# Optimization experiments

Measured on AMD Instinct MI355X. Metric: run time of the kernel, lower is better.

The kernel has to match this reference:

```python
import jax, jax.numpy as jnp
import numpy as np

N_HEAD = 16
HEAD_SIZE = 1024
EMBED = 1024
MULTI_HEAD_SIZE = HEAD_SIZE // N_HEAD  # 64; used only as the softmax scale (source bug)
B, S = 4, 2048


def setup_inputs() -> dict:
    key = jax.random.key(0)
    k1, k2, k3, k4 = jax.random.split(key, 4)
    x = jax.random.normal(k1, (B, S, EMBED), dtype=jnp.float32)
    w_qkv = jax.random.normal(k2, (3 * HEAD_SIZE, EMBED), dtype=jnp.float32) * 0.02
    w_proj = jax.random.normal(k3, (EMBED, HEAD_SIZE), dtype=jnp.float32) * 0.02
    b_proj = jax.random.normal(k4, (EMBED,), dtype=jnp.float32) * 0.02
    return {"x": x, "w_qkv": w_qkv, "w_proj": w_proj, "b_proj": b_proj}


def reference(x, w_qkv, w_proj, b_proj):
    # Fused QKV projection (Linear, no bias): [B,S,E] @ [E,3H] -> split
    qkv = jnp.einsum("bse,he->bsh", x, w_qkv)  # [B,S,3H]
    q, k, v = jnp.split(qkv, 3, axis=-1)       # each [B,S,H]
    # Source's non-flash path: attention over FULL Head_size dim (not per-head),
    # scaled by sqrt(multi_head_size) -- reproduced faithfully.
    scale = 1.0 / np.sqrt(MULTI_HEAD_SIZE).astype(np.float32)
    scores = jnp.einsum("bqh,bkh->bqk", q, k) * scale  # [B,S,S]
    probs = jax.nn.softmax(scores, axis=-1)            # dropout = identity (eval)
    out = jnp.einsum("bqk,bkh->bqh", probs, v)         # [B,S,H]
    # Faithful scrambling reshape: transpose(1,2).contiguous().view(B,S,H)
    Bn, Sn, H = out.shape
    out = jnp.swapaxes(out, 1, 2).reshape(Bn, Sn, H)
    # Output projection + residual dropout (identity in eval)
    out = jnp.einsum("bsh,eh->bse", out, w_proj) + b_proj
    return out
```

## Files before the change

### kernel.cpp

```cpp
#include <hip/hip_runtime.h>


typedef float f32x4 __attribute__((ext_vector_type(4)));
typedef short bf16x8 __attribute__((ext_vector_type(8)));
typedef short bf16x4 __attribute__((ext_vector_type(4)));
typedef unsigned short u16;

__device__ inline u16 f2bf(float f) {
  union { float f; unsigned u; } x; x.f = f;
  unsigned r = x.u + 0x7fffu + ((x.u >> 16) & 1u);
  return (u16)(r >> 16);
}

__device__ inline void gload_lds16(const void* g, void* l) {
  __builtin_amdgcn_global_load_lds(
      (const __attribute__((address_space(1))) void*)g,
      (__attribute__((address_space(3))) void*)l, 16, 0, 0);
}

__global__ __launch_bounds__(256) void cvt_kernel(const float* __restrict__ in,
                                                  u16* __restrict__ out, int n8) {
  int i = blockIdx.x * 256 + threadIdx.x;
  if (i >= n8) return;
  f32x4 a = *(const f32x4*)&in[(long)i * 8];
  f32x4 b = *(const f32x4*)&in[(long)i * 8 + 4];
  bf16x8 o;
#pragma unroll
  for (int j = 0; j < 4; ++j) { o[j] = (short)f2bf(a[j]); o[4 + j] = (short)f2bf(b[j]); }
  *(bf16x8*)&out[(long)i * 8] = o;
}

__global__ __launch_bounds__(256) void transpose_v(const u16* __restrict__ qkvb,
                                                   u16* __restrict__ vT) {
  __shared__ u16 tile[64][72];
  const int t = threadIdx.x;
  const long b = blockIdx.z;
  const int k0 = blockIdx.x * 64, h0 = blockIdx.y * 64;
  const u16* v = qkvb + b * 2048 * 3072 + 2048;
#pragma unroll
  for (int i = 0; i < 2; ++i) {
    int s = i * 256 + t; int r = s >> 3, c = (s & 7) * 8;
    bf16x8 val = *(const bf16x8*)&v[(long)(k0 + r) * 3072 + h0 + c];
    *(bf16x8*)&tile[r][c] = val;
  }
  __syncthreads();
  u16* o = vT + b * 1024 * 2048;
#pragma unroll
  for (int i = 0; i < 2; ++i) {
    int s = i * 256 + t; int r = s >> 3, c = (s & 7) * 8;
    bf16x8 val;
#pragma unroll
    for (int j = 0; j < 8; ++j) val[j] = tile[c + j][r];
    *(bf16x8*)&o[(long)(h0 + r) * 2048 + k0 + c] = val;
  }
}

__global__ __launch_bounds__(256) void softmax_k(const float* __restrict__ S,
                                                 u16* __restrict__ P,
                                                 long sS, long sP) {
  const int t = threadIdx.x;
  const float* row = S + (long)blockIdx.z * sS + (long)blockIdx.x * 2048;
  u16* prow = P + (long)blockIdx.z * sP + (long)blockIdx.x * 2048;
  f32x4 v0 = *(const f32x4*)&row[t * 8];
  f32x4 v1 = *(const f32x4*)&row[t * 8 + 4];
  float m = v0[0];
#pragma unroll
  for (int j = 1; j < 4; ++j) m = fmaxf(m, v0[j]);
#pragma unroll
  for (int j = 0; j < 4; ++j) m = fmaxf(m, v1[j]);
#pragma unroll
  for (int o = 32; o; o >>= 1) m = fmaxf(m, __shfl_xor(m, o));
  __shared__ float red[8];
  if ((t & 63) == 0) red[t >> 6] = m;
  __syncthreads();
  m = fmaxf(fmaxf(red[0], red[1]), fmaxf(red[2], red[3]));
  const float C = 0.18033688011112042f;
  float e[8], s = 0.f;
#pragma unroll
  for (int j = 0; j < 4; ++j) { e[j] = exp2f((v0[j] - m) * C); s += e[j]; }
#pragma unroll
  for (int j = 0; j < 4; ++j) { e[4 + j] = exp2f((v1[j] - m) * C); s += e[4 + j]; }
#pragma unroll
  for (int o = 32; o; o >>= 1) s += __shfl_xor(s, o);
  if ((t & 63) == 0) red[4 + (t >> 6)] = s;
  __syncthreads();
  float inv = 1.f / (red[4] + red[5] + red[6] + red[7]);
  bf16x8 ov;
#pragma unroll
  for (int j = 0; j < 8; ++j) ov[j] = (short)f2bf(e[j] * inv);
  *(bf16x8*)&prow[t * 8] = ov;
}

template <int MODE, int BM>
__global__ __launch_bounds__(512, 2) void gemm9(const u16* __restrict__ A0, int lda, long sAz,
                                                const u16* __restrict__ B0, int ldb, long sBz,
                                                void* __restrict__ C0, int ldc, long sCz,
                                                const float* __restrict__ bias, int K) {
  constexpr int MR = BM / 32;
  constexpr int LA = BM / 128;
  extern __shared__ __align__(16) u16 smem[];
  u16* Ab = smem;
  u16* Bb = smem + 4 * BM * 32;
  const int t = threadIdx.x, lane = t & 63, wv = t >> 6;
  const int wr = wv >> 2, wc = wv & 3;
  const int fr = lane & 15, hi = lane >> 4;

  const int gx = gridDim.x, gy = gridDim.y;
  long L = ((long)blockIdx.z * gy + blockIdx.y) * gx + blockIdx.x;
  const long NB = (long)gx * gy * gridDim.z;
  if ((NB & 7) == 0) L = (L & 7) * (NB >> 3) + (L >> 3);
  const int bx = (int)(L % gx);
  const int by = (int)((L / gx) % gy);
  const int bz = (int)(L / ((long)gx * gy));

  const long row0 = (long)by * BM, col0 = (long)bx * 256;
  const u16* A = A0 + (long)bz * sAz;
  const u16* B = B0 + (long)bz * sBz;

  f32x4 acc[MR][4];
#pragma unroll
  for (int m = 0; m < MR; ++m)
#pragma unroll
    for (int n = 0; n < 4; ++n) acc[m][n] = (f32x4){0.f, 0.f, 0.f, 0.f};

  auto stA = [&](int buf, int ks, int k0) {
#pragma unroll
    for (int i = 0; i < LA; ++i) {
      const int l = i * 512 + t;
      const int r = l >> 2, sl = (l & 3) ^ (r & 3);
      gload_lds16(A + (row0 + r) * (long)lda + k0 + ks * 32 + sl * 8,
                  Ab + (buf * 2 + ks) * BM * 32 + (i * 512 + wv * 64) * 8);
    }
  };
  auto stB = [&](int buf, int ks, int k0) {
#pragma unroll
    for (int i = 0; i < 2; ++i) {
      const int l = i * 512 + t;
      const int r = l >> 2, sl = (l & 3) ^ (r & 3);
      gload_lds16(B + (col0 + r) * (long)ldb + k0 + ks * 32 + sl * 8,
                  Bb + (buf * 2 + ks) * 256 * 32 + (i * 512 + wv * 64) * 8);
    }
  };
  auto aAddr = [&](int buf, int ks, int m) -> const u16* {
    const int r = wr * (BM / 2) + m * 16 + fr;
    return Ab + ((buf * 2 + ks) * BM + r) * 32 + (hi ^ (fr & 3)) * 8;
  };
  auto bAddr = [&](int buf, int ks, int n) -> const u16* {
    const int r = wc * 64 + n * 16 + fr;
    return Bb + ((buf * 2 + ks) * 256 + r) * 32 + (hi ^ (fr & 3)) * 8;
  };

  stA(0, 0, 0); stB(0, 0, 0);
  stA(0, 1, 0); stB(0, 1, 0);

  const int NT = K >> 6;
  for (int kt = 0; kt < NT; ++kt) {
    const int buf = kt & 1;
    const int kn = (kt + 1) << 6;
    const bool pf = (kt + 1 < NT);
#pragma unroll
    for (int ks = 0; ks < 2; ++ks) {
      if constexpr (LA == 2) asm volatile("s_waitcnt vmcnt(4)" ::: "memory");
      else                   asm volatile("s_waitcnt vmcnt(3)" ::: "memory");
      __builtin_amdgcn_s_barrier();
      __builtin_amdgcn_sched_barrier(0);
      bf16x8 afr[MR], b01[2], b23[2];
#pragma unroll
      for (int m = 0; m < MR; ++m) afr[m] = *(const bf16x8*)aAddr(buf, ks, m);
#pragma unroll
      for (int n = 0; n < 2; ++n) b01[n] = *(const bf16x8*)bAddr(buf, ks, n);
#pragma unroll
      for (int n = 0; n < 2; ++n) b23[n] = *(const bf16x8*)bAddr(buf, ks, 2 + n);
      if (pf) { stA(buf ^ 1, ks, kn); stB(buf ^ 1, ks, kn); }
      asm volatile("s_waitcnt lgkmcnt(2)" ::: "memory");
      __builtin_amdgcn_sched_barrier(0);
      __builtin_amdgcn_s_setprio(1);
#pragma unroll
      for (int m = 0; m < MR; ++m) {
        acc[m][0] = __builtin_amdgcn_mfma_f32_16x16x32_bf16(afr[m], b01[0], acc[m][0], 0, 0, 0);
        acc[m][1] = __builtin_amdgcn_mfma_f32_16x16x32_bf16(afr[m], b01[1], acc[m][1], 0, 0, 0);
      }
      __builtin_amdgcn_s_setprio(0);
      asm volatile("s_waitcnt lgkmcnt(0)" ::: "memory");
      __builtin_amdgcn_sched_barrier(0);
      __builtin_amdgcn_s_setprio(1);
#pragma unroll
      for (int m = 0; m < MR; ++m) {
        acc[m][2] = __builtin_amdgcn_mfma_f32_16x16x32_bf16(afr[m], b23[0], acc[m][2], 0, 0, 0);
        acc[m][3] = __builtin_amdgcn_mfma_f32_16x16x32_bf16(afr[m], b23[1], acc[m][3], 0, 0, 0);
      }
      __builtin_amdgcn_s_setprio(0);
    }
  }

#pragma unroll
  for (int m = 0; m < MR; ++m)
#pragma unroll
    for (int n = 0; n < 4; ++n) {
      const long r0 = row0 + wr * (BM / 2) + m * 16 + hi * 4;
      const long c = col0 + wc * 64 + n * 16 + fr;
      if (MODE == 0) {
        float* C = (float*)C0 + (long)bz * sCz;
#pragma unroll
        for (int j = 0; j < 4; ++j) C[(r0 + j) * ldc + c] = acc[m][n][j];
      } else if (MODE == 1) {
        u16* C = (u16*)C0 + (long)bz * sCz;
#pragma unroll
        for (int j = 0; j < 4; ++j) C[(r0 + j) * ldc + c] = f2bf(acc[m][n][j]);
      } else if (MODE == 2) {
        u16* C = (u16*)C0 + (long)bz * sCz;
        const int q0 = (int)r0;
        const long dr = 2 * c + (q0 >> 10);
        bf16x4 pk;
#pragma unroll
        for (int j = 0; j < 4; ++j) pk[j] = (short)f2bf(acc[m][n][j]);
        *(bf16x4*)&C[dr * 1024 + (q0 & 1023)] = pk;
      } else {
        float* C = (float*)C0 + (long)bz * sCz;
        const float bv = bias[c];
#pragma unroll
        for (int j = 0; j < 4; ++j) C[(r0 + j) * ldc + c] = acc[m][n][j] + bv;
      }
    }
}

extern "C" void kernel_launch(void* const* d_in, const int* in_sizes, int n_in,
                              void* d_out, int out_size, void* d_ws, size_t ws_size,
                              hipStream_t stream) {
  const float* x      = (const float*)d_in[0];
  const float* w_qkv  = (const float*)d_in[1];
  const float* w_proj = (const float*)d_in[2];
  const float* b_proj = (const float*)d_in[3];
  float* out = (float*)d_out;
  char* ws = (char*)d_ws;

  u16*   xb     = (u16*)(ws + 0);
  u16*   wqkvb  = (u16*)(ws + 16777216);
  u16*   wprojb = (u16*)(ws + 23068672);
  u16*   qkvb   = (u16*)(ws + 25165824);
  u16*   vT     = (u16*)(ws + 75497472);
  u16*   out2   = (u16*)(ws + 92274688);
  float* scores = (float*)(ws + 109051904);
  const bool full = ws_size >= 209715200ull;
  u16* probs = (u16*)(ws + (full ? 176160768 : 125829120));

  const int LDS128 = (4 * 128 * 32 + 4 * 256 * 32) * 2;
  const int LDS256 = (4 * 256 * 32 + 4 * 256 * 32) * 2;
  hipFuncSetAttribute((const void*)gemm9<1, 128>, hipFuncAttributeMaxDynamicSharedMemorySize, LDS128);
  hipFuncSetAttribute((const void*)gemm9<0, 256>, hipFuncAttributeMaxDynamicSharedMemorySize, LDS256);
  hipFuncSetAttribute((const void*)gemm9<2, 128>, hipFuncAttributeMaxDynamicSharedMemorySize, LDS128);
  hipFuncSetAttribute((const void*)gemm9<3, 128>, hipFuncAttributeMaxDynamicSharedMemorySize, LDS128);

  cvt_kernel<<<4096, 256, 0, stream>>>(x, xb, 1048576);
  cvt_kernel<<<1536, 256, 0, stream>>>(w_qkv, wqkvb, 393216);
  cvt_kernel<<<512, 256, 0, stream>>>(w_proj, wprojb, 131072);

  gemm9<1, 128><<<dim3(12, 64, 1), 512, LDS128, stream>>>(xb, 1024, 0, wqkvb, 1024, 0,
                                                          qkvb, 3072, 0, nullptr, 1024);
  transpose_v<<<dim3(32, 16, 4), 256, 0, stream>>>(qkvb, vT);

  const long sQ = 2048L * 3072;
  if (full) {
    gemm9<0, 256><<<dim3(8, 8, 4), 512, LDS256, stream>>>(qkvb, 3072, sQ, qkvb + 1024, 3072, sQ,
                                                          scores, 2048, 2048L * 2048, nullptr, 1024);
    softmax_k<<<dim3(2048, 1, 4), 256, 0, stream>>>(scores, probs, 2048L * 2048, 2048L * 2048);
    gemm9<2, 128><<<dim3(4, 16, 4), 512, LDS128, stream>>>(probs, 2048, 2048L * 2048, vT, 2048, 2048L * 1024,
                                                           out2, 1024, 2048L * 1024, nullptr, 2048);
  } else {
    for (int b = 0; b < 4; ++b) {
      const u16* qb = qkvb + (long)b * sQ;
      gemm9<0, 256><<<dim3(8, 8, 1), 512, LDS256, stream>>>(qb, 3072, 0, qb + 1024, 3072, 0,
                                                            scores, 2048, 0, nullptr, 1024);
      softmax_k<<<dim3(2048, 1, 1), 256, 0, stream>>>(scores, probs, 0, 0);
      gemm9<2, 128><<<dim3(4, 16, 1), 512, LDS128, stream>>>(probs, 2048, 0, vT + (long)b * 2048 * 1024, 2048, 0,
                                                             out2 + (long)b * 2048 * 1024, 1024, 0, nullptr, 2048);
    }
  }

  gemm9<3, 128><<<dim3(4, 64, 1), 512, LDS128, stream>>>(out2, 1024, 0, wprojb, 1024, 0,
                                                         out, 1024, 0, b_proj, 1024);
}
```

Before: 295.3 us.

## Simplify GEMM main loop to single-stage K=32 with higher occupancy

Replaces the hand-scheduled two-substep K=64 pipeline with a simpler K=32 double-buffered loop using __syncthreads, drops the XOR LDS swizzle, halves LDS per block, and raises the launch-bounds occupancy hint (4 or 6 waves-groups). The QKV GEMM also moves to a 256-row tile. The aim is more concurrent blocks to hide latency instead of explicit waitcnt/setprio scheduling, at the risk of LDS bank conflicts from the unswizzled layout and more barriers per K step.

```diff
diff --git a/kernel.cpp b/kernel.cpp
--- a/kernel.cpp
+++ b/kernel.cpp
@@ -91,16 +91,16 @@
   *(bf16x8*)&prow[t * 8] = ov;
 }
 
-template <int MODE, int BM>
-__global__ __launch_bounds__(512, 2) void gemm9(const u16* __restrict__ A0, int lda, long sAz,
-                                                const u16* __restrict__ B0, int ldb, long sBz,
-                                                void* __restrict__ C0, int ldc, long sCz,
-                                                const float* __restrict__ bias, int K) {
+template <int MODE, int BM, int MINW>
+__global__ __launch_bounds__(512, MINW) void gemm10(const u16* __restrict__ A0, int lda, long sAz,
+                                                    const u16* __restrict__ B0, int ldb, long sBz,
+                                                    void* __restrict__ C0, int ldc, long sCz,
+                                                    const float* __restrict__ bias, int K) {
   constexpr int MR = BM / 32;
   constexpr int LA = BM / 128;
   extern __shared__ __align__(16) u16 smem[];
   u16* Ab = smem;
-  u16* Bb = smem + 4 * BM * 32;
+  u16* Bb = smem + 2 * BM * 32;
   const int t = threadIdx.x, lane = t & 63, wv = t >> 6;
   const int wr = wv >> 2, wc = wv & 3;
   const int fr = lane & 15, hi = lane >> 4;
@@ -123,74 +123,43 @@
 #pragma unroll
     for (int n = 0; n < 4; ++n) acc[m][n] = (f32x4){0.f, 0.f, 0.f, 0.f};
 
-  auto stA = [&](int buf, int ks, int k0) {
+  auto stage = [&](int buf, int k0) {
 #pragma unroll
     for (int i = 0; i < LA; ++i) {
       const int l = i * 512 + t;
-      const int r = l >> 2, sl = (l & 3) ^ (r & 3);
-      gload_lds16(A + (row0 + r) * (long)lda + k0 + ks * 32 + sl * 8,
-                  Ab + (buf * 2 + ks) * BM * 32 + (i * 512 + wv * 64) * 8);
-    }
-  };
-  auto stB = [&](int buf, int ks, int k0) {
+      const int r = l >> 2, sl = l & 3;
+      gload_lds16(A + (row0 + r) * (long)lda + k0 + sl * 8,
+                  Ab + buf * BM * 32 + (i * 512 + wv * 64) * 8);
+    }
 #pragma unroll
     for (int i = 0; i < 2; ++i) {
       const int l = i * 512 + t;
-      const int r = l >> 2, sl = (l & 3) ^ (r & 3);
-      gload_lds16(B + (col0 + r) * (long)ldb + k0 + ks * 32 + sl * 8,
-                  Bb + (buf * 2 + ks) * 256 * 32 + (i * 512 + wv * 64) * 8);
+      const int r = l >> 2, sl = l & 3;
+      gload_lds16(B + (col0 + r) * (long)ldb + k0 + sl * 8,
+                  Bb + buf * 256 * 32 + (i * 512 + wv * 64) * 8);
     }
   };
-  auto aAddr = [&](int buf, int ks, int m) -> const u16* {
-    const int r = wr * (BM / 2) + m * 16 + fr;
-    return Ab + ((buf * 2 + ks) * BM + r) * 32 + (hi ^ (fr & 3)) * 8;
-  };
-  auto bAddr = [&](int buf, int ks, int n) -> const u16* {
-    const int r = wc * 64 + n * 16 + fr;
-    return Bb + ((buf * 2 + ks) * 256 + r) * 32 + (hi ^ (fr & 3)) * 8;
-  };
-
-  stA(0, 0, 0); stB(0, 0, 0);
-  stA(0, 1, 0); stB(0, 1, 0);
-
-  const int NT = K >> 6;
+
+  stage(0, 0);
+  __syncthreads();
+
+  const int NT = K >> 5;
   for (int kt = 0; kt < NT; ++kt) {
-    const int buf = kt & 1;
-    const int kn = (kt + 1) << 6;
-    const bool pf = (kt + 1 < NT);
-#pragma unroll
-    for (int ks = 0; ks < 2; ++ks) {
-      if constexpr (LA == 2) asm volatile("s_waitcnt vmcnt(4)" ::: "memory");
-      else                   asm volatile("s_waitcnt vmcnt(3)" ::: "memory");
-      __builtin_amdgcn_s_barrier();
-      __builtin_amdgcn_sched_barrier(0);
-      bf16x8 afr[MR], b01[2], b23[2];
-#pragma unroll
-      for (int m = 0; m < MR; ++m) afr[m] = *(const bf16x8*)aAddr(buf, ks, m);
-#pragma unroll
-      for (int n = 0; n < 2; ++n) b01[n] = *(const bf16x8*)bAddr(buf, ks, n);
-#pragma unroll
-      for (int n = 0; n < 2; ++n) b23[n] = *(const bf16x8*)bAddr(buf, ks, 2 + n);
-      if (pf) { stA(buf ^ 1, ks, kn); stB(buf ^ 1, ks, kn); }
-      asm volatile("s_waitcnt lgkmcnt(2)" ::: "memory");
-      __builtin_amdgcn_sched_barrier(0);
-      __builtin_amdgcn_s_setprio(1);
-#pragma unroll
-      for (int m = 0; m < MR; ++m) {
-        acc[m][0] = __builtin_amdgcn_mfma_f32_16x16x32_bf16(afr[m], b01[0], acc[m][0], 0, 0, 0);
-        acc[m][1] = __builtin_amdgcn_mfma_f32_16x16x32_bf16(afr[m], b01[1], acc[m][1], 0, 0, 0);
-      }
-      __builtin_amdgcn_s_setprio(0);
-      asm volatile("s_waitcnt lgkmcnt(0)" ::: "memory");
-      __builtin_amdgcn_sched_barrier(0);
-      __builtin_amdgcn_s_setprio(1);
-#pragma unroll
-      for (int m = 0; m < MR; ++m) {
-        acc[m][2] = __builtin_amdgcn_mfma_f32_16x16x32_bf16(afr[m], b23[0], acc[m][2], 0, 0, 0);
-        acc[m][3] = __builtin_amdgcn_mfma_f32_16x16x32_bf16(afr[m], b23[1], acc[m][3], 0, 0, 0);
-      }
-      __builtin_amdgcn_s_setprio(0);
-    }
+    const int cur = kt & 1;
+    if (kt + 1 < NT) stage(cur ^ 1, (kt + 1) << 5);
+    bf16x8 afr[MR], bfr[4];
+#pragma unroll
+    for (int m = 0; m < MR; ++m)
+      afr[m] = *(const bf16x8*)(Ab + (cur * BM + wr * (BM / 2) + m * 16 + fr) * 32 + hi * 8);
+#pragma unroll
+    for (int n = 0; n < 4; ++n)
+      bfr[n] = *(const bf16x8*)(Bb + (cur * 256 + wc * 64 + n * 16 + fr) * 32 + hi * 8);
+#pragma unroll
+    for (int m = 0; m < MR; ++m)
+#pragma unroll
+      for (int n = 0; n < 4; ++n)
+        acc[m][n] = __builtin_amdgcn_mfma_f32_16x16x32_bf16(afr[m], bfr[n], acc[m][n], 0, 0, 0);
+    __syncthreads();
   }
 
 #pragma unroll
@@ -244,39 +213,39 @@
   const bool full = ws_size >= 209715200ull;
   u16* probs = (u16*)(ws + (full ? 176160768 : 125829120));
 
-  const int LDS128 = (4 * 128 * 32 + 4 * 256 * 32) * 2;
-  const int LDS256 = (4 * 256 * 32 + 4 * 256 * 32) * 2;
-  hipFuncSetAttribute((const void*)gemm9<1, 128>, hipFuncAttributeMaxDynamicSharedMemorySize, LDS128);
-  hipFuncSetAttribute((const void*)gemm9<0, 256>, hipFuncAttributeMaxDynamicSharedMemorySize, LDS256);
-  hipFuncSetAttribute((const void*)gemm9<2, 128>, hipFuncAttributeMaxDynamicSharedMemorySize, LDS128);
-  hipFuncSetAttribute((const void*)gemm9<3, 128>, hipFuncAttributeMaxDynamicSharedMemorySize, LDS128);
+  const int L256 = (2 * 256 * 32 + 2 * 256 * 32) * 2;
+  const int L128 = (2 * 128 * 32 + 2 * 256 * 32) * 2;
+  hipFuncSetAttribute((const void*)gemm10<1, 256, 4>, hipFuncAttributeMaxDynamicSharedMemorySize, L256);
+  hipFuncSetAttribute((const void*)gemm10<0, 256, 4>, hipFuncAttributeMaxDynamicSharedMemorySize, L256);
+  hipFuncSetAttribute((const void*)gemm10<2, 128, 6>, hipFuncAttributeMaxDynamicSharedMemorySize, L128);
+  hipFuncSetAttribute((const void*)gemm10<3, 128, 6>, hipFuncAttributeMaxDynamicSharedMemorySize, L128);
 
   cvt_kernel<<<4096, 256, 0, stream>>>(x, xb, 1048576);
   cvt_kernel<<<1536, 256, 0, stream>>>(w_qkv, wqkvb, 393216);
   cvt_kernel<<<512, 256, 0, stream>>>(w_proj, wprojb, 131072);
 
-  gemm9<1, 128><<<dim3(12, 64, 1), 512, LDS128, stream>>>(xb, 1024, 0, wqkvb, 1024, 0,
-                                                          qkvb, 3072, 0, nullptr, 1024);
+  gemm10<1, 256, 4><<<dim3(12, 32, 1), 512, L256, stream>>>(xb, 1024, 0, wqkvb, 1024, 0,
+                                                            qkvb, 3072, 0, nullptr, 1024);
   transpose_v<<<dim3(32, 16, 4), 256, 0, stream>>>(qkvb, vT);
 
   const long sQ = 2048L * 3072;
   if (full) {
-    gemm9<0, 256><<<dim3(8, 8, 4), 512, LDS256, stream>>>(qkvb, 3072, sQ, qkvb + 1024, 3072, sQ,
-                                                          scores, 2048, 2048L * 2048, nullptr, 1024);
+    gemm10<0, 256, 4><<<dim3(8, 8, 4), 512, L256, stream>>>(qkvb, 3072, sQ, qkvb + 1024, 3072, sQ,
+                                                            scores, 2048, 2048L * 2048, nullptr, 1024);
     softmax_k<<<dim3(2048, 1, 4), 256, 0, stream>>>(scores, probs, 2048L * 2048, 2048L * 2048);
-    gemm9<2, 128><<<dim3(4, 16, 4), 512, LDS128, stream>>>(probs, 2048, 2048L * 2048, vT, 2048, 2048L * 1024,
-                                                           out2, 1024, 2048L * 1024, nullptr, 2048);
+    gemm10<2, 128, 6><<<dim3(4, 16, 4), 512, L128, stream>>>(probs, 2048, 2048L * 2048, vT, 2048, 2048L * 1024,
+                                                             out2, 1024, 2048L * 1024, nullptr, 2048);
   } else {
     for (int b = 0; b < 4; ++b) {
       const u16* qb = qkvb + (long)b * sQ;
-      gemm9<0, 256><<<dim3(8, 8, 1), 512, LDS256, stream>>>(qb, 3072, 0, qb + 1024, 3072, 0,
-                                                            scores, 2048, 0, nullptr, 1024);
+      gemm10<0, 256, 4><<<dim3(8, 8, 1), 512, L256, stream>>>(qb, 3072, 0, qb + 1024, 3072, 0,
+                                                              scores, 2048, 0, nullptr, 1024);
       softmax_k<<<dim3(2048, 1, 1), 256, 0, stream>>>(scores, probs, 0, 0);
-      gemm9<2, 128><<<dim3(4, 16, 1), 512, LDS128, stream>>>(probs, 2048, 0, vT + (long)b * 2048 * 1024, 2048, 0,
-                                                             out2 + (long)b * 2048 * 1024, 1024, 0, nullptr, 2048);
-    }
-  }
-
-  gemm9<3, 128><<<dim3(4, 64, 1), 512, LDS128, stream>>>(out2, 1024, 0, wprojb, 1024, 0,
-                                                         out, 1024, 0, b_proj, 1024);
-}
+      gemm10<2, 128, 6><<<dim3(4, 16, 1), 512, L128, stream>>>(probs, 2048, 0, vT + (long)b * 2048 * 1024, 2048, 0,
+                                                               out2 + (long)b * 2048 * 1024, 1024, 0, nullptr, 2048);
+    }
+  }
+
+  gemm10<3, 128, 6><<<dim3(4, 64, 1), 512, L128, stream>>>(out2, 1024, 0, wprojb, 1024, 0,
+                                                           out, 1024, 0, b_proj, 1024);
+}
```

After: 912.5 us. +209.0%, slower.
